# Kernel optimization log

Measured on AMD Instinct MI355X. Metric: run time of the kernel, lower is better.

Reference implementation:

```python
import jax, jax.numpy as jnp
import numpy as np

N_NODES = 50000
N_EDGES = 640000
D_IN = 128
D_HID = 256
D_OUT = 128


def _linear_params(key, d_in, d_out):
    kw, kb = jax.random.split(key)
    bound = 1.0 / np.sqrt(d_in)
    W = jax.random.uniform(kw, (d_in, d_out), jnp.float32, -bound, bound)
    b = jax.random.uniform(kb, (d_out,), jnp.float32, -bound, bound)
    return W, b


def setup_inputs() -> dict:
    key = jax.random.key(0)
    ks = jax.random.split(key, 6)
    x = jax.random.normal(ks[0], (N_NODES, D_IN), jnp.float32)
    edge_index = jax.random.randint(ks[1], (2, N_EDGES), 0, N_NODES, jnp.int64)
    W1a, b1a = _linear_params(ks[2], D_IN, D_HID)
    W1b, b1b = _linear_params(ks[3], D_HID, D_HID)
    W2a, b2a = _linear_params(ks[4], D_HID, D_HID)
    W2b, b2b = _linear_params(ks[5], D_HID, D_OUT)
    return {"x": x, "edge_index": edge_index,
            "W1a": W1a, "b1a": b1a, "W1b": W1b, "b1b": b1b,
            "W2a": W2a, "b2a": b2a, "W2b": W2b, "b2b": b2b}


def _gin_conv(x, src, dst, Wa, ba, Wb, bb):
    # sum-aggregate neighbor features: agg[i] = sum_{(j->i) in E} x[j]
    agg = jax.ops.segment_sum(x[src], dst, num_segments=N_NODES)
    h = x + agg  # (1 + eps) * x + agg, eps = 0 (PyG default)
    h = jnp.maximum(h @ Wa + ba, 0.0)  # Linear + ReLU
    return h @ Wb + bb                 # Linear


def reference(x, edge_index, W1a, b1a, W1b, b1b, W2a, b2a, W2b, b2b):
    src, dst = edge_index[0], edge_index[1]
    h = _gin_conv(x, src, dst, W1a, b1a, W1b, b1b)
    h = jnp.maximum(h, 0.0)  # ReLU; dropout is identity in eval mode
    return _gin_conv(h, src, dst, W2a, b2a, W2b, b2b)
```

## Files before the change

kernel.cpp:

```cpp
#include <hip/hip_runtime.h>

#define N_NODES 50000
#define N_EDGES 640000
#define PADROWS 50048
#define SLOTS   48

typedef __attribute__((ext_vector_type(8))) short bf16x8;
typedef __attribute__((ext_vector_type(4))) float f32x4;

__device__ inline ushort rne16(float f) {
    unsigned u = __builtin_bit_cast(unsigned, f);
    unsigned r = u + 0x7fffu + ((u >> 16) & 1u);
    return (ushort)(r >> 16);
}
__device__ inline float b2f(ushort h) {
    return __builtin_bit_cast(float, (unsigned)h << 16);
}

__device__ inline void glds16(const ushort* g, ushort* l) {
    __builtin_amdgcn_global_load_lds(
        (const __attribute__((address_space(1))) void*)g,
        (__attribute__((address_space(3))) void*)l, 16, 0, 0);
}


__global__ __launch_bounds__(256) void scatter_slot(const int* __restrict__ src,
                                                    const int* __restrict__ dst,
                                                    int* __restrict__ cnt,
                                                    int* __restrict__ elist) {
    int e = blockIdx.x * 256 + threadIdx.x;
    if (e < N_EDGES) {
        unsigned d = (unsigned)dst[e];
        unsigned s = (unsigned)src[e];
        if (d < N_NODES && s < N_NODES) {
            int pos = atomicAdd(&cnt[d], 1);
            if (pos < SLOTS) elist[(size_t)d * SLOTS + pos] = (int)s;
        }
    }
}

__global__ __launch_bounds__(256) void decomp_all(const float* __restrict__ W1a,
                                                  const float* __restrict__ W1b,
                                                  const float* __restrict__ W2a,
                                                  const float* __restrict__ W2b,
                                                  ushort* __restrict__ o1a,
                                                  ushort* __restrict__ o1b,
                                                  ushort* __restrict__ o2a,
                                                  ushort* __restrict__ o2b) {
    int b = blockIdx.x;
    const float* W; ushort* O; int K, N, base;
    if (b < 128)      { W = W1a; O = o1a; K = 128; N = 256; base = 0; }
    else if (b < 384) { W = W1b; O = o1b; K = 256; N = 256; base = 128; }
    else if (b < 640) { W = W2a; O = o2a; K = 256; N = 256; base = 384; }
    else              { W = W2b; O = o2b; K = 256; N = 128; base = 640; }
    int idx = (b - base) * 256 + threadIdx.x;
    int n = idx / K, k = idx - n * K;
    O[idx] = rne16(W[(size_t)k * N + n]);
}

__global__ __launch_bounds__(256) void round_x(const float* __restrict__ x,
                                               ushort* __restrict__ xb) {
    int i = blockIdx.x * 256 + threadIdx.x;
    if (i >= N_NODES * 128 / 4) return;
    float4 v = ((const float4*)x)[i];
    ushort4 o = make_ushort4(rne16(v.x), rne16(v.y), rne16(v.z), rne16(v.w));
    ((ushort4*)xb)[i] = o;
}

__global__ __launch_bounds__(256) void agg_x(const float* __restrict__ x,
                                             const ushort* __restrict__ xb,
                                             const int* __restrict__ cnt,
                                             const int* __restrict__ elist,
                                             ushort* __restrict__ h0b) {
    const int l = threadIdx.x & 31;
    const int node = blockIdx.x * 8 + (threadIdx.x >> 5);
    if (node >= N_NODES) return;
    float4 s4 = ((const float4*)(x + (size_t)node * 128))[l];
    float a0 = s4.x, a1 = s4.y, a2 = s4.z, a3 = s4.w;
    float c0 = 0.f, c1 = 0.f, c2 = 0.f, c3 = 0.f;
    int n = cnt[node]; if (n > SLOTS) n = SLOTS;
    const int* el = elist + (size_t)node * SLOTS;
    int i = 0;
    for (; i + 2 <= n; i += 2) {
        ushort4 v0 = ((const ushort4*)(xb + (size_t)el[i] * 128))[l];
        ushort4 v1 = ((const ushort4*)(xb + (size_t)el[i + 1] * 128))[l];
        a0 += b2f(v0.x); a1 += b2f(v0.y); a2 += b2f(v0.z); a3 += b2f(v0.w);
        c0 += b2f(v1.x); c1 += b2f(v1.y); c2 += b2f(v1.z); c3 += b2f(v1.w);
    }
    if (i < n) {
        ushort4 v = ((const ushort4*)(xb + (size_t)el[i] * 128))[l];
        a0 += b2f(v.x); a1 += b2f(v.y); a2 += b2f(v.z); a3 += b2f(v.w);
    }
    a0 += c0; a1 += c1; a2 += c2; a3 += c3;
    ushort4 o = make_ushort4(rne16(a0), rne16(a1), rne16(a2), rne16(a3));
    ((ushort4*)(h0b + (size_t)node * 128))[l] = o;
}

__global__ __launch_bounds__(256) void agg_h(const ushort* __restrict__ hBb,
                                             const int* __restrict__ cnt,
                                             const int* __restrict__ elist,
                                             ushort* __restrict__ hCb) {
    const int l = threadIdx.x & 63;
    const int node = blockIdx.x * 4 + (threadIdx.x >> 6);
    if (node >= N_NODES) return;
    ushort4 s4 = ((const ushort4*)(hBb + (size_t)node * 256))[l];
    float a0 = b2f(s4.x), a1 = b2f(s4.y), a2 = b2f(s4.z), a3 = b2f(s4.w);
    float c0 = 0.f, c1 = 0.f, c2 = 0.f, c3 = 0.f;
    int n = cnt[node]; if (n > SLOTS) n = SLOTS;
    const int* el = elist + (size_t)node * SLOTS;
    int i = 0;
    for (; i + 2 <= n; i += 2) {
        ushort4 v0 = ((const ushort4*)(hBb + (size_t)el[i] * 256))[l];
        ushort4 v1 = ((const ushort4*)(hBb + (size_t)el[i + 1] * 256))[l];
        a0 += b2f(v0.x); a1 += b2f(v0.y); a2 += b2f(v0.z); a3 += b2f(v0.w);
        c0 += b2f(v1.x); c1 += b2f(v1.y); c2 += b2f(v1.z); c3 += b2f(v1.w);
    }
    if (i < n) {
        ushort4 v = ((const ushort4*)(hBb + (size_t)el[i] * 256))[l];
        a0 += b2f(v.x); a1 += b2f(v.y); a2 += b2f(v.z); a3 += b2f(v.w);
    }
    a0 += c0; a1 += c1; a2 += c2; a3 += c3;
    ushort4 o = make_ushort4(rne16(a0), rne16(a1), rne16(a2), rne16(a3));
    ((ushort4*)(hCb + (size_t)node * 256))[l] = o;
}


template <int K1, int N2, bool RELU2, bool BF16OUT>
__global__ __launch_bounds__(256, 2) void fused_mlp(const ushort* __restrict__ Ag,
                                                    const ushort* __restrict__ W1g,
                                                    const float* __restrict__ b1,
                                                    const ushort* __restrict__ W2g,
                                                    const float* __restrict__ b2,
                                                    float* __restrict__ Cf,
                                                    ushort* __restrict__ Cb,
                                                    int M) {
    constexpr int NI2 = N2 / 32;
    __shared__ ushort bufA[64 * 64];
    __shared__ ushort bufB[256 * 64];
    __shared__ ushort C1[64 * 256];
    const int tid = threadIdx.x;
    const int lane = tid & 63;
    const int wid = tid >> 6;
    const int wm = wid >> 1, wn = wid & 1;
    const int row0 = blockIdx.x * 64;
    const int stB = lane >> 3;
    const int kel = (((lane & 7) << 4) ^ (stB << 4)) >> 1;

    f32x4 acc1[2][8];
#pragma unroll
    for (int i = 0; i < 2; ++i)
#pragma unroll
        for (int j = 0; j < 8; ++j) acc1[i][j] = (f32x4){0.f, 0.f, 0.f, 0.f};

    for (int k0 = 0; k0 < K1; k0 += 64) {
#pragma unroll
        for (int i = 0; i < 10; ++i) {
            int t = i * 4 + wid;
            if (t < 8) glds16(Ag + (size_t)(row0 + t * 8 + stB) * K1 + k0 + kel, bufA + t * 512);
            else       glds16(W1g + (size_t)((t - 8) * 8 + stB) * K1 + k0 + kel, bufB + (t - 8) * 512);
        }
        __syncthreads();
#pragma unroll
        for (int ki = 0; ki < 2; ++ki) {
            const int kb = ki * 64 + ((lane >> 4) << 4);
            bf16x8 a[2], b[8];
#pragma unroll
            for (int mi = 0; mi < 2; ++mi) {
                int row = wm * 32 + mi * 16 + (lane & 15);
                int off = (row * 128 + kb) ^ ((row & 7) << 4);
                a[mi] = *(const bf16x8*)((const char*)bufA + off);
            }
#pragma unroll
            for (int ni = 0; ni < 8; ++ni) {
                int col = wn * 128 + ni * 16 + (lane & 15);
                int off = (col * 128 + kb) ^ ((col & 7) << 4);
                b[ni] = *(const bf16x8*)((const char*)bufB + off);
            }
#pragma unroll
            for (int mi = 0; mi < 2; ++mi)
#pragma unroll
                for (int ni = 0; ni < 8; ++ni)
                    acc1[mi][ni] = __builtin_amdgcn_mfma_f32_16x16x32_bf16(a[mi], b[ni], acc1[mi][ni], 0, 0, 0);
        }
        __syncthreads();
    }
#pragma unroll
    for (int ni = 0; ni < 8; ++ni) {
        int col = wn * 128 + ni * 16 + (lane & 15);
        float bv = b1[col];
#pragma unroll
        for (int mi = 0; mi < 2; ++mi) {
            int rowb = wm * 32 + mi * 16 + ((lane >> 4) << 2);
            f32x4 av = acc1[mi][ni];
#pragma unroll
            for (int r = 0; r < 4; ++r) {
                int row = rowb + r;
                int off = (row * 512 + col * 2) ^ ((row & 7) << 4);
                *(ushort*)((char*)C1 + off) = rne16(fmaxf(av[r] + bv, 0.f));
            }
        }
    }

    f32x4 acc2[2][NI2];
#pragma unroll
    for (int i = 0; i < 2; ++i)
#pragma unroll
        for (int j = 0; j < NI2; ++j) acc2[i][j] = (f32x4){0.f, 0.f, 0.f, 0.f};

    for (int k0 = 0; k0 < 256; k0 += 64) {
#pragma unroll
        for (int i = 0; i < N2 / 32; ++i) {
            int t = i * 4 + wid;
            glds16(W2g + (size_t)(t * 8 + stB) * 256 + k0 + kel, bufB + t * 512);
        }
        __syncthreads();
#pragma unroll
        for (int ki = 0; ki < 2; ++ki) {
            const int kb = ki * 64 + ((lane >> 4) << 4);
            bf16x8 a[2], b[NI2];
#pragma unroll
            for (int mi = 0; mi < 2; ++mi) {
                int row = wm * 32 + mi * 16 + (lane & 15);
                int off = (row * 512 + k0 * 2 + kb) ^ ((row & 7) << 4);
                a[mi] = *(const bf16x8*)((const char*)C1 + off);
            }
#pragma unroll
            for (int ni = 0; ni < NI2; ++ni) {
                int col = wn * (N2 / 2) + ni * 16 + (lane & 15);
                int off = (col * 128 + kb) ^ ((col & 7) << 4);
                b[ni] = *(const bf16x8*)((const char*)bufB + off);
            }
#pragma unroll
            for (int mi = 0; mi < 2; ++mi)
#pragma unroll
                for (int ni = 0; ni < NI2; ++ni)
                    acc2[mi][ni] = __builtin_amdgcn_mfma_f32_16x16x32_bf16(a[mi], b[ni], acc2[mi][ni], 0, 0, 0);
        }
        __syncthreads();
    }
#pragma unroll
    for (int ni = 0; ni < NI2; ++ni) {
        int col = wn * (N2 / 2) + ni * 16 + (lane & 15);
        float bv = b2[col];
#pragma unroll
        for (int mi = 0; mi < 2; ++mi) {
            int rowb = row0 + wm * 32 + mi * 16 + ((lane >> 4) << 2);
            f32x4 av = acc2[mi][ni];
#pragma unroll
            for (int r = 0; r < 4; ++r) {
                int row = rowb + r;
                if (row < M) {
                    float f = av[r] + bv;
                    if (RELU2) f = fmaxf(f, 0.f);
                    if (BF16OUT) Cb[(size_t)row * N2 + col] = rne16(f);
                    else         Cf[(size_t)row * N2 + col] = f;
                }
            }
        }
    }
}


extern "C" void kernel_launch(void* const* d_in, const int* in_sizes, int n_in,
                              void* d_out, int out_size, void* d_ws, size_t ws_size,
                              hipStream_t stream) {
    const float* x   = (const float*)d_in[0];
    const int*   ei  = (const int*)d_in[1];
    const float* W1a = (const float*)d_in[2];
    const float* b1a = (const float*)d_in[3];
    const float* W1b = (const float*)d_in[4];
    const float* b1b = (const float*)d_in[5];
    const float* W2a = (const float*)d_in[6];
    const float* b2a = (const float*)d_in[7];
    const float* W2b = (const float*)d_in[8];
    const float* b2b = (const float*)d_in[9];
    float* out = (float*)d_out;

    const int* src = ei;
    const int* dst = ei + N_EDGES;

    int* cnt   = (int*)d_ws;
    int* elist = cnt + N_NODES;

    size_t ob = (((size_t)(N_NODES + (size_t)N_NODES * SLOTS) * 4) + 255) & ~(size_t)255;
    ushort* w1a = (ushort*)((char*)d_ws + ob);
    ushort* w1b = w1a + 256 * 128;
    ushort* w2a = w1b + 256 * 256;
    ushort* w2b = w2a + 256 * 256;
    char*   wend = (char*)(w2b + 128 * 256);

    size_t fb = ((size_t)(wend - (char*)d_ws) + 255) & ~(size_t)255;
    const size_t P128 = (size_t)PADROWS * 128;
    const size_t P256 = (size_t)PADROWS * 256;
    ushort* xb  = (ushort*)((char*)d_ws + fb);
    ushort* h0b = xb  + P128;
    ushort* hBb = h0b + P128;
    ushort* hCb = hBb + P256;

    hipMemsetAsync(cnt, 0, (size_t)N_NODES * sizeof(int), stream);

    const int eb = (N_EDGES + 255) / 256;
    scatter_slot<<<eb, 256, 0, stream>>>(src, dst, cnt, elist);

    decomp_all<<<768, 256, 0, stream>>>(W1a, W1b, W2a, W2b, w1a, w1b, w2a, w2b);
    round_x<<<(N_NODES * 128 / 4 + 255) / 256, 256, 0, stream>>>(x, xb);

    const int gb = PADROWS / 64;
    agg_x<<<(N_NODES + 7) / 8, 256, 0, stream>>>(x, xb, cnt, elist, h0b);
    fused_mlp<128, 256, true, true><<<gb, 256, 0, stream>>>(
        h0b, w1a, b1a, w1b, b1b, nullptr, hBb, N_NODES);
    agg_h<<<(N_NODES + 3) / 4, 256, 0, stream>>>(hBb, cnt, elist, hCb);
    fused_mlp<256, 128, false, false><<<gb, 256, 0, stream>>>(
        hCb, w2a, b2a, w2b, b2b, out, nullptr, N_NODES);
}
```

Measured before the change: 201.6 us.

## Fuse neighbor aggregation into MLP kernel, gathering rows directly into LDS

Removes the separate agg_x and agg_h kernels. Each fused_gin block now gathers and sums neighbor rows for its 64 nodes straight into a swizzled LDS A tile, then runs the two GEMMs, so the aggregated intermediate no longer makes a global-memory round trip. The block grows to 512 threads as a 2x4 wave grid. The first layer's self term now comes from the bf16-rounded x instead of fp32 x, which slightly changes the numerics. The larger shared A tile (64xK1) together with launch_bounds(512,1) may reduce occupancy and limit latency hiding for the irregular gathers.

```diff
diff --git a/kernel.cpp b/kernel.cpp
--- a/kernel.cpp
+++ b/kernel.cpp
@@ -15,6 +15,12 @@
 }
 __device__ inline float b2f(ushort h) {
     return __builtin_bit_cast(float, (unsigned)h << 16);
+}
+__device__ inline void unp8add(float* a, uint4 v) {
+    a[0] += b2f((ushort)v.x); a[1] += b2f((ushort)(v.x >> 16));
+    a[2] += b2f((ushort)v.y); a[3] += b2f((ushort)(v.y >> 16));
+    a[4] += b2f((ushort)v.z); a[5] += b2f((ushort)(v.z >> 16));
+    a[6] += b2f((ushort)v.w); a[7] += b2f((ushort)(v.w >> 16));
 }
 
 __device__ inline void glds16(const ushort* g, ushort* l) {
@@ -67,66 +73,11 @@
     ((ushort4*)xb)[i] = o;
 }
 
-__global__ __launch_bounds__(256) void agg_x(const float* __restrict__ x,
-                                             const ushort* __restrict__ xb,
-                                             const int* __restrict__ cnt,
-                                             const int* __restrict__ elist,
-                                             ushort* __restrict__ h0b) {
-    const int l = threadIdx.x & 31;
-    const int node = blockIdx.x * 8 + (threadIdx.x >> 5);
-    if (node >= N_NODES) return;
-    float4 s4 = ((const float4*)(x + (size_t)node * 128))[l];
-    float a0 = s4.x, a1 = s4.y, a2 = s4.z, a3 = s4.w;
-    float c0 = 0.f, c1 = 0.f, c2 = 0.f, c3 = 0.f;
-    int n = cnt[node]; if (n > SLOTS) n = SLOTS;
-    const int* el = elist + (size_t)node * SLOTS;
-    int i = 0;
-    for (; i + 2 <= n; i += 2) {
-        ushort4 v0 = ((const ushort4*)(xb + (size_t)el[i] * 128))[l];
-        ushort4 v1 = ((const ushort4*)(xb + (size_t)el[i + 1] * 128))[l];
-        a0 += b2f(v0.x); a1 += b2f(v0.y); a2 += b2f(v0.z); a3 += b2f(v0.w);
-        c0 += b2f(v1.x); c1 += b2f(v1.y); c2 += b2f(v1.z); c3 += b2f(v1.w);
-    }
-    if (i < n) {
-        ushort4 v = ((const ushort4*)(xb + (size_t)el[i] * 128))[l];
-        a0 += b2f(v.x); a1 += b2f(v.y); a2 += b2f(v.z); a3 += b2f(v.w);
-    }
-    a0 += c0; a1 += c1; a2 += c2; a3 += c3;
-    ushort4 o = make_ushort4(rne16(a0), rne16(a1), rne16(a2), rne16(a3));
-    ((ushort4*)(h0b + (size_t)node * 128))[l] = o;
-}
-
-__global__ __launch_bounds__(256) void agg_h(const ushort* __restrict__ hBb,
-                                             const int* __restrict__ cnt,
-                                             const int* __restrict__ elist,
-                                             ushort* __restrict__ hCb) {
-    const int l = threadIdx.x & 63;
-    const int node = blockIdx.x * 4 + (threadIdx.x >> 6);
-    if (node >= N_NODES) return;
-    ushort4 s4 = ((const ushort4*)(hBb + (size_t)node * 256))[l];
-    float a0 = b2f(s4.x), a1 = b2f(s4.y), a2 = b2f(s4.z), a3 = b2f(s4.w);
-    float c0 = 0.f, c1 = 0.f, c2 = 0.f, c3 = 0.f;
-    int n = cnt[node]; if (n > SLOTS) n = SLOTS;
-    const int* el = elist + (size_t)node * SLOTS;
-    int i = 0;
-    for (; i + 2 <= n; i += 2) {
-        ushort4 v0 = ((const ushort4*)(hBb + (size_t)el[i] * 256))[l];
-        ushort4 v1 = ((const ushort4*)(hBb + (size_t)el[i + 1] * 256))[l];
-        a0 += b2f(v0.x); a1 += b2f(v0.y); a2 += b2f(v0.z); a3 += b2f(v0.w);
-        c0 += b2f(v1.x); c1 += b2f(v1.y); c2 += b2f(v1.z); c3 += b2f(v1.w);
-    }
-    if (i < n) {
-        ushort4 v = ((const ushort4*)(hBb + (size_t)el[i] * 256))[l];
-        a0 += b2f(v.x); a1 += b2f(v.y); a2 += b2f(v.z); a3 += b2f(v.w);
-    }
-    a0 += c0; a1 += c1; a2 += c2; a3 += c3;
-    ushort4 o = make_ushort4(rne16(a0), rne16(a1), rne16(a2), rne16(a3));
-    ((ushort4*)(hCb + (size_t)node * 256))[l] = o;
-}
-
 
 template <int K1, int N2, bool RELU2, bool BF16OUT>
-__global__ __launch_bounds__(256, 2) void fused_mlp(const ushort* __restrict__ Ag,
+__global__ __launch_bounds__(512, 1) void fused_gin(const ushort* __restrict__ Ag,
+                                                    const int* __restrict__ cnt,
+                                                    const int* __restrict__ elist,
                                                     const ushort* __restrict__ W1g,
                                                     const float* __restrict__ b1,
                                                     const ushort* __restrict__ W2g,
@@ -134,59 +85,103 @@
                                                     float* __restrict__ Cf,
                                                     ushort* __restrict__ Cb,
                                                     int M) {
-    constexpr int NI2 = N2 / 32;
-    __shared__ ushort bufA[64 * 64];
-    __shared__ ushort bufB[256 * 64];
+    constexpr int RS = K1 * 2;
+    constexpr int NI2 = N2 / 64;
+    __shared__ ushort At[64 * K1];
+    __shared__ ushort Bt[256 * 64];
     __shared__ ushort C1[64 * 256];
     const int tid = threadIdx.x;
     const int lane = tid & 63;
     const int wid = tid >> 6;
-    const int wm = wid >> 1, wn = wid & 1;
+    const int wm = wid >> 2, wn = wid & 3;
     const int row0 = blockIdx.x * 64;
     const int stB = lane >> 3;
     const int kel = (((lane & 7) << 4) ^ (stB << 4)) >> 1;
 
-    f32x4 acc1[2][8];
+    constexpr int LPR = K1 / 8;
+    constexpr int RPW = 64 / LPR;
+    const int lg = lane % LPR;
+    const int lr = lane / LPR;
+#pragma unroll
+    for (int p = 0; p < 8 / RPW; ++p) {
+        const int row = wid * 8 + p * RPW + lr;
+        const int grow = row0 + row;
+        float a0[8] = {0,0,0,0,0,0,0,0};
+        float c1[8] = {0,0,0,0,0,0,0,0};
+        float c2[8] = {0,0,0,0,0,0,0,0};
+        float c3[8] = {0,0,0,0,0,0,0,0};
+        int deg = 0;
+        const int* el = elist;
+        if (grow < N_NODES) {
+            uint4 sv = *(const uint4*)(Ag + (size_t)grow * K1 + lg * 8);
+            unp8add(a0, sv);
+            deg = cnt[grow]; if (deg > SLOTS) deg = SLOTS;
+            el = elist + (size_t)grow * SLOTS;
+        }
+        int i = 0;
+        for (; i + 4 <= deg; i += 4) {
+            uint4 v0 = *(const uint4*)(Ag + (size_t)el[i]     * K1 + lg * 8);
+            uint4 v1 = *(const uint4*)(Ag + (size_t)el[i + 1] * K1 + lg * 8);
+            uint4 v2 = *(const uint4*)(Ag + (size_t)el[i + 2] * K1 + lg * 8);
+            uint4 v3 = *(const uint4*)(Ag + (size_t)el[i + 3] * K1 + lg * 8);
+            unp8add(a0, v0); unp8add(c1, v1); unp8add(c2, v2); unp8add(c3, v3);
+        }
+        for (; i < deg; ++i) {
+            uint4 v = *(const uint4*)(Ag + (size_t)el[i] * K1 + lg * 8);
+            unp8add(a0, v);
+        }
+#pragma unroll
+        for (int j = 0; j < 8; ++j) a0[j] += c1[j] + c2[j] + c3[j];
+        uint4 pw;
+        pw.x = rne16(a0[0]) | ((unsigned)rne16(a0[1]) << 16);
+        pw.y = rne16(a0[2]) | ((unsigned)rne16(a0[3]) << 16);
+        pw.z = rne16(a0[4]) | ((unsigned)rne16(a0[5]) << 16);
+        pw.w = rne16(a0[6]) | ((unsigned)rne16(a0[7]) << 16);
+        int off = (row * RS + lg * 16) ^ ((row & 7) << 4);
+        *(uint4*)((char*)At + off) = pw;
+    }
+    __syncthreads();
+
+    f32x4 acc1[2][4];
 #pragma unroll
     for (int i = 0; i < 2; ++i)
 #pragma unroll
-        for (int j = 0; j < 8; ++j) acc1[i][j] = (f32x4){0.f, 0.f, 0.f, 0.f};
+        for (int j = 0; j < 4; ++j) acc1[i][j] = (f32x4){0.f, 0.f, 0.f, 0.f};
 
     for (int k0 = 0; k0 < K1; k0 += 64) {
 #pragma unroll
-        for (int i = 0; i < 10; ++i) {
-            int t = i * 4 + wid;
-            if (t < 8) glds16(Ag + (size_t)(row0 + t * 8 + stB) * K1 + k0 + kel, bufA + t * 512);
-            else       glds16(W1g + (size_t)((t - 8) * 8 + stB) * K1 + k0 + kel, bufB + (t - 8) * 512);
+        for (int i = 0; i < 4; ++i) {
+            int t = i * 8 + wid;
+            glds16(W1g + (size_t)(t * 8 + stB) * K1 + k0 + kel, Bt + t * 512);
         }
         __syncthreads();
 #pragma unroll
         for (int ki = 0; ki < 2; ++ki) {
             const int kb = ki * 64 + ((lane >> 4) << 4);
-            bf16x8 a[2], b[8];
+            bf16x8 a[2], b[4];
 #pragma unroll
             for (int mi = 0; mi < 2; ++mi) {
                 int row = wm * 32 + mi * 16 + (lane & 15);
-                int off = (row * 128 + kb) ^ ((row & 7) << 4);
-                a[mi] = *(const bf16x8*)((const char*)bufA + off);
-            }
-#pragma unroll
-            for (int ni = 0; ni < 8; ++ni) {
-                int col = wn * 128 + ni * 16 + (lane & 15);
+                int off = (row * RS + k0 * 2 + kb) ^ ((row & 7) << 4);
+                a[mi] = *(const bf16x8*)((const char*)At + off);
+            }
+#pragma unroll
+            for (int ni = 0; ni < 4; ++ni) {
+                int col = wn * 64 + ni * 16 + (lane & 15);
                 int off = (col * 128 + kb) ^ ((col & 7) << 4);
-                b[ni] = *(const bf16x8*)((const char*)bufB + off);
+                b[ni] = *(const bf16x8*)((const char*)Bt + off);
             }
 #pragma unroll
             for (int mi = 0; mi < 2; ++mi)
 #pragma unroll
-                for (int ni = 0; ni < 8; ++ni)
+                for (int ni = 0; ni < 4; ++ni)
                     acc1[mi][ni] = __builtin_amdgcn_mfma_f32_16x16x32_bf16(a[mi], b[ni], acc1[mi][ni], 0, 0, 0);
         }
         __syncthreads();
     }
 #pragma unroll
-    for (int ni = 0; ni < 8; ++ni) {
-        int col = wn * 128 + ni * 16 + (lane & 15);
+    for (int ni = 0; ni < 4; ++ni) {
+        int col = wn * 64 + ni * 16 + (lane & 15);
         float bv = b1[col];
 #pragma unroll
         for (int mi = 0; mi < 2; ++mi) {
@@ -209,9 +204,9 @@
 
     for (int k0 = 0; k0 < 256; k0 += 64) {
 #pragma unroll
-        for (int i = 0; i < N2 / 32; ++i) {
-            int t = i * 4 + wid;
-            glds16(W2g + (size_t)(t * 8 + stB) * 256 + k0 + kel, bufB + t * 512);
+        for (int i = 0; i < N2 / 64; ++i) {
+            int t = i * 8 + wid;
+            glds16(W2g + (size_t)(t * 8 + stB) * 256 + k0 + kel, Bt + t * 512);
         }
         __syncthreads();
 #pragma unroll
@@ -226,9 +221,9 @@
             }
 #pragma unroll
             for (int ni = 0; ni < NI2; ++ni) {
-                int col = wn * (N2 / 2) + ni * 16 + (lane & 15);
+                int col = wn * (N2 / 4) + ni * 16 + (lane & 15);
                 int off = (col * 128 + kb) ^ ((col & 7) << 4);
-                b[ni] = *(const bf16x8*)((const char*)bufB + off);
+                b[ni] = *(const bf16x8*)((const char*)Bt + off);
             }
 #pragma unroll
             for (int mi = 0; mi < 2; ++mi)
@@ -240,7 +235,7 @@
     }
 #pragma unroll
     for (int ni = 0; ni < NI2; ++ni) {
-        int col = wn * (N2 / 2) + ni * 16 + (lane & 15);
+        int col = wn * (N2 / 4) + ni * 16 + (lane & 15);
         float bv = b2[col];
 #pragma unroll
         for (int mi = 0; mi < 2; ++mi) {
@@ -291,11 +286,8 @@
 
     size_t fb = ((size_t)(wend - (char*)d_ws) + 255) & ~(size_t)255;
     const size_t P128 = (size_t)PADROWS * 128;
-    const size_t P256 = (size_t)PADROWS * 256;
     ushort* xb  = (ushort*)((char*)d_ws + fb);
-    ushort* h0b = xb  + P128;
-    ushort* hBb = h0b + P128;
-    ushort* hCb = hBb + P256;
+    ushort* hBb = xb + P128;
 
     hipMemsetAsync(cnt, 0, (size_t)N_NODES * sizeof(int), stream);
 
@@ -306,10 +298,8 @@
     round_x<<<(N_NODES * 128 / 4 + 255) / 256, 256, 0, stream>>>(x, xb);
 
     const int gb = PADROWS / 64;
-    agg_x<<<(N_NODES + 7) / 8, 256, 0, stream>>>(x, xb, cnt, elist, h0b);
-    fused_mlp<128, 256, true, true><<<gb, 256, 0, stream>>>(
-        h0b, w1a, b1a, w1b, b1b, nullptr, hBb, N_NODES);
-    agg_h<<<(N_NODES + 3) / 4, 256, 0, stream>>>(hBb, cnt, elist, hCb);
-    fused_mlp<256, 128, false, false><<<gb, 256, 0, stream>>>(
-        hCb, w2a, b2a, w2b, b2b, out, nullptr, N_NODES);
-}
+    fused_gin<128, 256, true, true><<<gb, 512, 0, stream>>>(
+        xb, cnt, elist, w1a, b1a, w1b, b1b, nullptr, hBb, N_NODES);
+    fused_gin<256, 128, false, false><<<gb, 512, 0, stream>>>(
+        hBb, cnt, elist, w2a, b2a, w2b, b2b, out, nullptr, N_NODES);
+}
```

After: 224.0 us. 1.11x slower.
